# Performance work log

Measured on AMD Instinct MI355X. Metric: run time of the kernel, lower is better.

The kernel has to match this reference:

```python
import jax, jax.numpy as jnp
import numpy as np

N, C, W_DIM, H_DIM = 2, 256, 64, 64
HEADS = 4
DH = C // HEADS  # per-head dim for Q,K,V projections
EPS = 1e-5


def _layernorm(x, w, b):
    mu = jnp.mean(x, axis=-1, keepdims=True)
    var = jnp.var(x, axis=-1, keepdims=True)
    return (x - mu) * jax.lax.rsqrt(var + EPS) * w + b


def setup_inputs() -> dict:
    key = jax.random.key(0)
    ks = jax.random.split(key, 12)
    s = 1.0 / np.sqrt(C)
    return {
        "x": jax.random.normal(ks[0], (N, C, W_DIM, H_DIM), dtype=jnp.float32),
        "ln1_w": jnp.ones((C,), jnp.float32),
        "ln1_b": jnp.zeros((C,), jnp.float32),
        # per-head projection weights, laid out for x @ W: [heads, C, DH]
        "WQ": jax.random.normal(ks[1], (HEADS, C, DH), jnp.float32) * s,
        "WK": jax.random.normal(ks[2], (HEADS, C, DH), jnp.float32) * s,
        "WV": jax.random.normal(ks[3], (HEADS, C, DH), jnp.float32) * s,
        "ln2_w": jnp.ones((C,), jnp.float32),
        "ln2_b": jnp.zeros((C,), jnp.float32),
        "W1": jax.random.normal(ks[4], (C, C), jnp.float32) * s,
        "b1": jnp.zeros((C,), jnp.float32),
        "W2": jax.random.normal(ks[5], (C, C), jnp.float32) * s,
        "b2": jnp.zeros((C,), jnp.float32),
    }


def reference(x, ln1_w, ln1_b, WQ, WK, WV, ln2_w, ln2_b, W1, b1, W2, b2):
    n, c, w, h = x.shape
    s = w * h
    # 'n c w h -> n (w h) c'
    r = x.reshape(n, c, s).transpose(0, 2, 1)          # [n, s, c]
    norm = _layernorm(r, ln1_w, ln1_b)
    # all heads at once (original loops over heads)
    Q = jnp.einsum('nsc,hcd->nhsd', norm, WQ)
    K = jnp.einsum('nsc,hcd->nhsd', norm, WK)
    V = jnp.einsum('nsc,hcd->nhsd', norm, WV)
    # scale is 1/sqrt(seq_len) per original (keys.shape[1])
    y = jnp.einsum('nhqd,nhkd->nhqk', Q, K) / jnp.sqrt(jnp.float32(s))
    # QUIRK: softmax over dim=1 of [n, q, k] => the QUERY axis (axis=2 here)
    z = jax.nn.softmax(y, axis=2)
    attn = jnp.einsum('nhqk,nhkd->nhqd', z, V)         # [n, h, s, dh]
    attn_cat = attn.transpose(0, 2, 1, 3).reshape(n, s, c)
    out = attn_cat + r
    out = _layernorm(out, ln2_w, ln2_b)
    out = jax.nn.gelu(out @ W1 + b1, approximate=False) @ W2 + b2
    out = out + attn_cat
    # 'n (w h) c -> n c w h'
    return out.transpose(0, 2, 1).reshape(n, c, w, h)
```

## Files before the change

kernel.cpp:

```cpp
#include <hip/hip_runtime.h>
#include <math.h>

#define SEQ 4096
#define CH  256
#define NHT 8
#define DHD 64

#define QSCALE 0.0225421092f

using bf16x8 = __attribute__((ext_vector_type(8))) short;
using f32x4  = __attribute__((ext_vector_type(4))) float;
typedef unsigned short u16;
typedef unsigned int   u32;

__device__ __forceinline__ u16 f2bf(float f) {
    u32 u = __float_as_uint(f);
    u = (u + 0x7fffu + ((u >> 16) & 1u)) >> 16;
    return (u16)u;
}
__device__ __forceinline__ float bf2f(u16 h) {
    return __uint_as_float(((u32)h) << 16);
}
__device__ __forceinline__ float fexp2(float x) {
    return __builtin_amdgcn_exp2f(x);
}

__global__ __launch_bounds__(256) void k_prep(const float* __restrict__ x,
                                              const float* __restrict__ ln1w,
                                              const float* __restrict__ ln1b,
                                              const float* __restrict__ WQ,
                                              const float* __restrict__ WK,
                                              const float* __restrict__ WV,
                                              const float* __restrict__ W1,
                                              const float* __restrict__ W2,
                                              u16* __restrict__ norm,
                                              u16* __restrict__ BtQKV,
                                              u16* __restrict__ W1t,
                                              u16* __restrict__ W2t)
{
    __shared__ float tile[32][257];
    __shared__ float mu[32], rs[32];
    int bid = blockIdx.x;
    int t = threadIdx.x;
    if (bid < 1280) {
        int id = bid * 256 + t;
        if (id < 768 * 256) {
            int j = id >> 8, c = id & 255;
            int which = j >> 8, h = (j >> 6) & 3, d = j & 63;
            const float* W = (which == 0) ? WQ : (which == 1) ? WK : WV;
            BtQKV[id] = f2bf(W[(h * 256 + c) * 64 + d]);
        } else if (id < 768 * 256 + 65536) {
            int jj = id - 768 * 256;
            int j = jj >> 8, c = jj & 255;
            W1t[jj] = f2bf(W1[c * 256 + j]);
        } else if (id < 768 * 256 + 2 * 65536) {
            int jj = id - 768 * 256 - 65536;
            int j = jj >> 8, c = jj & 255;
            W2t[jj] = f2bf(W2[c * 256 + j]);
        }
        return;
    }
    int b2i = bid - 1280;
    int n = b2i >> 7, s0 = (b2i & 127) * 32;
    int sl = t & 31, cg = t >> 5;
    for (int cc = 0; cc < 256; cc += 8) {
        int c = cc + cg;
        tile[sl][c] = x[(n * 256 + c) * SEQ + s0 + sl];
    }
    __syncthreads();
    int wv = t >> 6, l = t & 63;
    for (int rr = 0; rr < 8; rr++) {
        int s = wv * 8 + rr;
        float a0 = tile[s][l], a1 = tile[s][l + 64], a2 = tile[s][l + 128], a3 = tile[s][l + 192];
        float sm = a0 + a1 + a2 + a3;
        float sq = a0 * a0 + a1 * a1 + a2 * a2 + a3 * a3;
        for (int off = 32; off; off >>= 1) { sm += __shfl_xor(sm, off); sq += __shfl_xor(sq, off); }
        if (l == 0) {
            float m = sm * (1.f / 256.f);
            mu[s] = m;
            rs[s] = rsqrtf(sq * (1.f / 256.f) - m * m + 1e-5f);
        }
    }
    __syncthreads();
    float ww = ln1w[t], bb = ln1b[t];
    for (int s = 0; s < 32; s++) {
        float v = (tile[s][t] - mu[s]) * rs[s] * ww + bb;
        norm[(n * SEQ + s0 + s) * 256 + t] = f2bf(v);
    }
}

__global__ __launch_bounds__(256) void k_qkv(const u16* __restrict__ norm,
                                             const u16* __restrict__ Bt,
                                             u16* __restrict__ Qo,
                                             u16* __restrict__ Ko,
                                             u16* __restrict__ Vto)
{
    int m0 = blockIdx.x * 64, j0 = blockIdx.y * 128;
    int t = threadIdx.x, w = t >> 6, lane = t & 63, quad = lane >> 4, l16 = lane & 15;
    const u16* Ap = norm + (long)(m0 + w * 16 + l16) * 256;
    const u16* Bp = Bt + (long)j0 * 256;
    f32x4 z = {0.f, 0.f, 0.f, 0.f};
    f32x4 acc[8];
    #pragma unroll
    for (int j = 0; j < 8; j++) acc[j] = z;
    #pragma unroll
    for (int kc = 0; kc < 8; kc++) {
        bf16x8 a = *(const bf16x8*)&Ap[kc * 32 + quad * 8];
        #pragma unroll
        for (int j = 0; j < 8; j++) {
            bf16x8 b = *(const bf16x8*)&Bp[(long)(j * 16 + l16) * 256 + kc * 32 + quad * 8];
            acc[j] = __builtin_amdgcn_mfma_f32_16x16x32_bf16(a, b, acc[j], 0, 0, 0);
        }
    }
    #pragma unroll
    for (int j = 0; j < 8; j++) {
        int col = j0 + j * 16 + l16;
        int which = col >> 8, h = (col >> 6) & 3, d = col & 63;
        int m = m0 + w * 16 + quad * 4;
        int n = m >> 12, s = m & 4095;
        if (which == 2) {
            u16 h0 = f2bf(acc[j][0]), h1 = f2bf(acc[j][1]);
            u16 h2_ = f2bf(acc[j][2]), h3 = f2bf(acc[j][3]);
            uint2 pk;
            pk.x = (u32)h0 | ((u32)h1 << 16);
            pk.y = (u32)h2_ | ((u32)h3 << 16);
            *(uint2*)&Vto[((long)(n * 4 + h) * 64 + d) * SEQ + s] = pk;
        } else {
            u16* dst = (which == 0) ? Qo : Ko;
            float sc = (which == 0) ? QSCALE : 1.0f;
            #pragma unroll
            for (int r = 0; r < 4; r++)
                dst[((n * 4 + h) * SEQ + s + r) * 64 + d] = f2bf(acc[j][r] * sc);
        }
    }
}

__global__ __launch_bounds__(256) void k_pass1(const u16* __restrict__ Q,
                                               const u16* __restrict__ Km,
                                               float* __restrict__ D2)
{
    __shared__ float Dred[128];
    int nh = blockIdx.y, k0 = blockIdx.x * 128, qc = blockIdx.z;
    const u16* Qh = Q + (long)nh * SEQ * 64;
    const u16* Kh = Km + (long)nh * SEQ * 64;
    int t = threadIdx.x, w = t >> 6, lane = t & 63, quad = lane >> 4, l16 = lane & 15;
    bf16x8 Kf[8][2];
    #pragma unroll
    for (int i = 0; i < 8; i++) {
        Kf[i][0] = *(const bf16x8*)&Kh[(k0 + i * 16 + l16) * 64 + quad * 8];
        Kf[i][1] = *(const bf16x8*)&Kh[(k0 + i * 16 + l16) * 64 + 32 + quad * 8];
    }
    if (t < 128) Dred[t] = 0.f;
    f32x4 z = {0.f, 0.f, 0.f, 0.f};
    float Dacc[8][4] = {};
    const int qw0 = qc * 2048 + w * 512;
    bf16x8 b0 = *(const bf16x8*)&Qh[(qw0 + l16) * 64 + quad * 8];
    bf16x8 b1 = *(const bf16x8*)&Qh[(qw0 + l16) * 64 + 32 + quad * 8];
    for (int step = 0; step < 32; step++) {
        int q = qw0 + step * 16;
        bf16x8 n0, n1;
        if (step < 31) {
            n0 = *(const bf16x8*)&Qh[(q + 16 + l16) * 64 + quad * 8];
            n1 = *(const bf16x8*)&Qh[(q + 16 + l16) * 64 + 32 + quad * 8];
        }
        #pragma unroll
        for (int i = 0; i < 8; i++) {
            f32x4 acc = z;
            acc = __builtin_amdgcn_mfma_f32_16x16x32_bf16(Kf[i][0], b0, acc, 0, 0, 0);
            acc = __builtin_amdgcn_mfma_f32_16x16x32_bf16(Kf[i][1], b1, acc, 0, 0, 0);
            #pragma unroll
            for (int r = 0; r < 4; r++) Dacc[i][r] += fexp2(acc[r]);
        }
        b0 = n0; b1 = n1;
    }
    #pragma unroll
    for (int i = 0; i < 8; i++)
        #pragma unroll
        for (int r = 0; r < 4; r++) {
            float v = Dacc[i][r];
            v += __shfl_xor(v, 1); v += __shfl_xor(v, 2);
            v += __shfl_xor(v, 4); v += __shfl_xor(v, 8);
            Dacc[i][r] = v;
        }
    __syncthreads();
    if (l16 == 0) {
        #pragma unroll
        for (int i = 0; i < 8; i++)
            #pragma unroll
            for (int r = 0; r < 4; r++)
                atomicAdd(&Dred[i * 16 + quad * 4 + r], Dacc[i][r]);
    }
    __syncthreads();
    if (t < 128) D2[((long)(qc * NHT + nh)) * SEQ + k0 + t] = Dred[t];
}

__global__ __launch_bounds__(256, 1) void k_pass2(const u16* __restrict__ Q,
                                                  const u16* __restrict__ Km,
                                                  const u16* __restrict__ Vt,
                                                  const float* __restrict__ D2,
                                                  float* __restrict__ acat2)
{
    __shared__ __align__(16) u16 lP[4][128][36];
    __shared__ float Lk[2048];
    float (*red)[68] = (float(*)[68])lP;

    int nh = blockIdx.y, q0 = blockIdx.x * 128, kcid = blockIdx.z;
    int n = nh >> 2, h = nh & 3;
    const u16* Qh = Q + (long)nh * SEQ * 64;
    const u16* Kh = Km + (long)nh * SEQ * 64;
    const u16* Vh = Vt + (long)nh * 64 * SEQ;
    int t = threadIdx.x, w = t >> 6, lane = t & 63, quad = lane >> 4, l16 = lane & 15;
    const int kw0 = kcid * 2048 + w * 512;
    const int klw = w * 512;

    {
        const float* Dp = D2 + (long)nh * SEQ + kcid * 2048;
        const long QS = (long)NHT * SEQ;
        #pragma unroll
        for (int off = 0; off < 8; off++) {
            int kl = off * 256 + t;
            Lk[kl] = __log2f(Dp[kl] + Dp[QS + kl]);
        }
    }
    bf16x8 Qf[8][2];
    #pragma unroll
    for (int jq = 0; jq < 8; jq++)
        #pragma unroll
        for (int ch = 0; ch < 2; ch++)
            Qf[jq][ch] = *(const bf16x8*)&Qh[(q0 + jq * 16 + l16) * 64 + ch * 32 + quad * 8];
    bf16x8 kA[2][2];
    #pragma unroll
    for (int ksub = 0; ksub < 2; ksub++) {
        kA[ksub][0] = *(const bf16x8*)&Kh[(kw0 + ksub * 16 + l16) * 64 + quad * 8];
        kA[ksub][1] = *(const bf16x8*)&Kh[(kw0 + ksub * 16 + l16) * 64 + 32 + quad * 8];
    }
    bf16x8 vb[4];
    #pragma unroll
    for (int jd = 0; jd < 4; jd++)
        vb[jd] = *(const bf16x8*)&Vh[(jd * 16 + l16) * SEQ + kw0 + quad * 8];
    f32x4 z = {0.f, 0.f, 0.f, 0.f};
    f32x4 accO[8][4];
    #pragma unroll
    for (int jq = 0; jq < 8; jq++)
        #pragma unroll
        for (int jd = 0; jd < 4; jd++) accO[jq][jd] = z;
    __syncthreads();

    for (int i = 0; i < 16; i++) {
        int k0 = kw0 + i * 32;
        #pragma unroll
        for (int ksub = 0; ksub < 2; ksub++) {
            f32x4 Lv = *(const f32x4*)&Lk[klw + i * 32 + ksub * 16 + quad * 4];
            #pragma unroll
            for (int jq = 0; jq < 8; jq++) {
                f32x4 acc = z;
                acc = __builtin_amdgcn_mfma_f32_16x16x32_bf16(kA[ksub][0], Qf[jq][0], acc, 0, 0, 0);
                acc = __builtin_amdgcn_mfma_f32_16x16x32_bf16(kA[ksub][1], Qf[jq][1], acc, 0, 0, 0);
                u32 e0 = __float_as_uint(fexp2(acc[0] - Lv[0]));
                u32 e1 = __float_as_uint(fexp2(acc[1] - Lv[1]));
                u32 e2 = __float_as_uint(fexp2(acc[2] - Lv[2]));
                u32 e3 = __float_as_uint(fexp2(acc[3] - Lv[3]));
                uint2 pk;
                pk.x = __builtin_amdgcn_perm(e1, e0, 0x07060302u);
                pk.y = __builtin_amdgcn_perm(e3, e2, 0x07060302u);
                *(uint2*)&lP[w][jq * 16 + l16][ksub * 16 + quad * 4] = pk;
            }
        }
        if (i < 15) {
            #pragma unroll
            for (int ksub = 0; ksub < 2; ksub++) {
                kA[ksub][0] = *(const bf16x8*)&Kh[(k0 + 32 + ksub * 16 + l16) * 64 + quad * 8];
                kA[ksub][1] = *(const bf16x8*)&Kh[(k0 + 32 + ksub * 16 + l16) * 64 + 32 + quad * 8];
            }
        }
        #pragma unroll
        for (int jq = 0; jq < 8; jq++) {
            bf16x8 pa = *(const bf16x8*)&lP[w][jq * 16 + l16][quad * 8];
            #pragma unroll
            for (int jd = 0; jd < 4; jd++)
                accO[jq][jd] = __builtin_amdgcn_mfma_f32_16x16x32_bf16(pa, vb[jd], accO[jq][jd], 0, 0, 0);
        }
        if (i < 15) {
            #pragma unroll
            for (int jd = 0; jd < 4; jd++)
                vb[jd] = *(const bf16x8*)&Vh[(jd * 16 + l16) * SEQ + k0 + 32 + quad * 8];
        }
    }
    __syncthreads();
    for (int src = 0; src < 4; src++) {
        if (w == src) {
            #pragma unroll
            for (int jq = 0; jq < 8; jq++)
                #pragma unroll
                for (int jd = 0; jd < 4; jd++)
                    #pragma unroll
                    for (int r = 0; r < 4; r++) {
                        float* cell = &red[jq * 16 + quad * 4 + r][jd * 16 + l16];
                        if (src == 0) *cell = accO[jq][jd][r];
                        else          *cell += accO[jq][jd][r];
                    }
        }
        __syncthreads();
    }
    float* dst = acat2 + (long)kcid * 8192 * 256;
    #pragma unroll
    for (int p = 0; p < 8; p++) {
        int row = p * 16 + (t >> 4);
        int ch = (t & 15) * 4;
        float4 o = *(float4*)&red[row][ch];
        *(float4*)&dst[((long)n * SEQ + q0 + row) * 256 + h * 64 + ch] = o;
    }
}

__global__ __launch_bounds__(256) void k_tail(const float* __restrict__ x,
                                              const float* __restrict__ acat2,
                                              const float* __restrict__ lnw,
                                              const float* __restrict__ lnb,
                                              const u16* __restrict__ W1t,
                                              const float* __restrict__ b1v,
                                              const u16* __restrict__ W2t,
                                              const float* __restrict__ b2v,
                                              float* __restrict__ out)
{
    __shared__ __align__(16) unsigned char smem[16448];
    float (*tile)[257] = (float(*)[257])smem;
    u16 (*lT)[264] = (u16(*)[264])smem;
    __shared__ float aF[16][257];
    __shared__ float mu[16], rs[16];
    __shared__ __align__(16) u16 lH[16][264];

    const long STRIDE = (long)8192 * 256;
    int m0 = blockIdx.x * 16;
    int n = m0 >> 12, s0 = m0 & 4095;
    int t = threadIdx.x, w = t >> 6, lane = t & 63, quad = lane >> 4, l16 = lane & 15;

    {
        int sl = t & 15, cg = t >> 4;
        for (int cc = 0; cc < 256; cc += 16) {
            int c = cc + cg;
            tile[sl][c] = x[(n * 256 + c) * SEQ + s0 + sl];
        }
    }
    __syncthreads();
    for (int s = 0; s < 16; s++) {
        long idx = (long)(m0 + s) * 256 + t;
        float a = acat2[idx] + acat2[idx + STRIDE];
        aF[s][t] = a;
        tile[s][t] += a;
    }
    __syncthreads();
    {
        int l = t & 63;
        for (int rr = 0; rr < 4; rr++) {
            int s = w * 4 + rr;
            float a0 = tile[s][l], a1 = tile[s][l + 64], a2 = tile[s][l + 128], a3 = tile[s][l + 192];
            float sm = a0 + a1 + a2 + a3;
            float sq = a0 * a0 + a1 * a1 + a2 * a2 + a3 * a3;
            for (int off = 32; off; off >>= 1) { sm += __shfl_xor(sm, off); sq += __shfl_xor(sq, off); }
            if (l == 0) {
                float m = sm * (1.f / 256.f);
                mu[s] = m;
                rs[s] = rsqrtf(sq * (1.f / 256.f) - m * m + 1e-5f);
            }
        }
    }
    __syncthreads();
    {
        float ww = lnw[t], bb = lnb[t];
        for (int s = 0; s < 16; s++)
            lH[s][t] = f2bf((tile[s][t] - mu[s]) * rs[s] * ww + bb);
    }
    __syncthreads();

    f32x4 z = {0.f, 0.f, 0.f, 0.f};
    f32x4 acc1[4];
    #pragma unroll
    for (int js = 0; js < 4; js++) acc1[js] = z;
    #pragma unroll
    for (int kc = 0; kc < 8; kc++) {
        bf16x8 b = *(const bf16x8*)&lH[l16][kc * 32 + quad * 8];
        #pragma unroll
        for (int js = 0; js < 4; js++) {
            bf16x8 a = *(const bf16x8*)&W1t[(long)(w * 64 + js * 16 + l16) * 256 + kc * 32 + quad * 8];
            acc1[js] = __builtin_amdgcn_mfma_f32_16x16x32_bf16(a, b, acc1[js], 0, 0, 0);
        }
    }
    #pragma unroll
    for (int js = 0; js < 4; js++) {
        u32 e[4];
        #pragma unroll
        for (int r = 0; r < 4; r++) {
            int j = w * 64 + js * 16 + quad * 4 + r;
            float v = acc1[js][r] + b1v[j];
            float g = 0.5f * v * (1.f + erff(v * 0.70710678118f));
            u32 u = __float_as_uint(g);
            e[r] = u + 0x7fffu + ((u >> 16) & 1u);
        }
        uint2 pk;
        pk.x = __builtin_amdgcn_perm(e[1], e[0], 0x07060302u);
        pk.y = __builtin_amdgcn_perm(e[3], e[2], 0x07060302u);
        *(uint2*)&lT[l16][w * 64 + js * 16 + quad * 4] = pk;
    }
    __syncthreads();
    f32x4 acc2[4];
    #pragma unroll
    for (int cs = 0; cs < 4; cs++) acc2[cs] = z;
    #pragma unroll
    for (int kc = 0; kc < 8; kc++) {
        bf16x8 pa = *(const bf16x8*)&lT[l16][kc * 32 + quad * 8];
        #pragma unroll
        for (int cs = 0; cs < 4; cs++) {
            bf16x8 wb = *(const bf16x8*)&W2t[(long)(w * 64 + cs * 16 + l16) * 256 + kc * 32 + quad * 8];
            acc2[cs] = __builtin_amdgcn_mfma_f32_16x16x32_bf16(pa, wb, acc2[cs], 0, 0, 0);
        }
    }
    #pragma unroll
    for (int cs = 0; cs < 4; cs++) {
        int c = w * 64 + cs * 16 + l16;
        float bj = b2v[c];
        float vv[4];
        #pragma unroll
        for (int r = 0; r < 4; r++)
            vv[r] = acc2[cs][r] + bj + aF[quad * 4 + r][c];
        float4 o = make_float4(vv[0], vv[1], vv[2], vv[3]);
        *(float4*)&out[((long)n * 256 + c) * SEQ + s0 + quad * 4] = o;
    }
}

extern "C" void kernel_launch(void* const* d_in, const int* in_sizes, int n_in,
                              void* d_out, int out_size, void* d_ws, size_t ws_size,
                              hipStream_t stream) {
    const float* x    = (const float*)d_in[0];
    const float* ln1w = (const float*)d_in[1];
    const float* ln1b = (const float*)d_in[2];
    const float* WQ   = (const float*)d_in[3];
    const float* WK   = (const float*)d_in[4];
    const float* WV   = (const float*)d_in[5];
    const float* ln2w = (const float*)d_in[6];
    const float* ln2b = (const float*)d_in[7];
    const float* W1   = (const float*)d_in[8];
    const float* b1   = (const float*)d_in[9];
    const float* W2   = (const float*)d_in[10];
    const float* b2   = (const float*)d_in[11];
    float* out = (float*)d_out;

    char* p = (char*)d_ws;
    u16* norm   = (u16*)p;   p += (size_t)8192 * 256 * 2;
    u16* BtQKV  = (u16*)p;   p += (size_t)768 * 256 * 2;
    u16* W1t    = (u16*)p;   p += (size_t)256 * 256 * 2;
    u16* W2t    = (u16*)p;   p += (size_t)256 * 256 * 2;
    u16* Qb     = (u16*)p;   p += (size_t)NHT * SEQ * 64 * 2;
    u16* Kb     = (u16*)p;   p += (size_t)NHT * SEQ * 64 * 2;
    u16* VtT    = (u16*)p;   p += (size_t)NHT * SEQ * 64 * 2;
    float* D2   = (float*)p; p += (size_t)2 * NHT * SEQ * 4;
    float* acat2= (float*)p; p += (size_t)2 * 8192 * 256 * 4;

    k_prep<<<1536, 256, 0, stream>>>(x, ln1w, ln1b, WQ, WK, WV, W1, W2,
                                     norm, BtQKV, W1t, W2t);
    k_qkv<<<dim3(128, 6), 256, 0, stream>>>(norm, BtQKV, Qb, Kb, VtT);
    k_pass1<<<dim3(32, 8, 2), 256, 0, stream>>>(Qb, Kb, D2);
    k_pass2<<<dim3(32, 8, 2), 256, 0, stream>>>(Qb, Kb, VtT, D2, acat2);
    k_tail<<<512, 256, 0, stream>>>(x, acat2, ln2w, ln2b, W1t, b1, W2t, b2, out);
}
```

Measured before the change: 232.1 us.

## Double-buffer P tile and software-pipeline QK/exp with PV MFMAs in pass2

Splits the per-wave P staging buffer in LDS into two buffers. The loop is restructured so the QK MFMA plus exp phase for step i+1 is issued before the PV MFMA phase for step i. This aims to overlap the exp2/pack VALU work and the LDS writes with independent matrix-core work, rather than serialising them within each step. The cost is doubled LDS use for P and a longer, fully unrolled code body.

```diff
diff --git a/kernel.cpp b/kernel.cpp
--- a/kernel.cpp
+++ b/kernel.cpp
@@ -200,9 +200,10 @@
                                                   const float* __restrict__ D2,
                                                   float* __restrict__ acat2)
 {
-    __shared__ __align__(16) u16 lP[4][128][36];
+    __shared__ __align__(16) u16 lPA[4][128][36];
+    __shared__ __align__(16) u16 lPB[4][128][36];
     __shared__ float Lk[2048];
-    float (*red)[68] = (float(*)[68])lP;
+    float (*red)[68] = (float(*)[68])lPA;
 
     int nh = blockIdx.y, q0 = blockIdx.x * 128, kcid = blockIdx.z;
     int n = nh >> 2, h = nh & 3;
@@ -246,46 +247,70 @@
         for (int jd = 0; jd < 4; jd++) accO[jq][jd] = z;
     __syncthreads();
 
-    for (int i = 0; i < 16; i++) {
-        int k0 = kw0 + i * 32;
-        #pragma unroll
-        for (int ksub = 0; ksub < 2; ksub++) {
-            f32x4 Lv = *(const f32x4*)&Lk[klw + i * 32 + ksub * 16 + quad * 4];
-            #pragma unroll
-            for (int jq = 0; jq < 8; jq++) {
-                f32x4 acc = z;
-                acc = __builtin_amdgcn_mfma_f32_16x16x32_bf16(kA[ksub][0], Qf[jq][0], acc, 0, 0, 0);
-                acc = __builtin_amdgcn_mfma_f32_16x16x32_bf16(kA[ksub][1], Qf[jq][1], acc, 0, 0, 0);
-                u32 e0 = __float_as_uint(fexp2(acc[0] - Lv[0]));
-                u32 e1 = __float_as_uint(fexp2(acc[1] - Lv[1]));
-                u32 e2 = __float_as_uint(fexp2(acc[2] - Lv[2]));
-                u32 e3 = __float_as_uint(fexp2(acc[3] - Lv[3]));
-                uint2 pk;
-                pk.x = __builtin_amdgcn_perm(e1, e0, 0x07060302u);
-                pk.y = __builtin_amdgcn_perm(e3, e2, 0x07060302u);
-                *(uint2*)&lP[w][jq * 16 + l16][ksub * 16 + quad * 4] = pk;
-            }
-        }
-        if (i < 15) {
-            #pragma unroll
-            for (int ksub = 0; ksub < 2; ksub++) {
-                kA[ksub][0] = *(const bf16x8*)&Kh[(k0 + 32 + ksub * 16 + l16) * 64 + quad * 8];
-                kA[ksub][1] = *(const bf16x8*)&Kh[(k0 + 32 + ksub * 16 + l16) * 64 + 32 + quad * 8];
-            }
-        }
-        #pragma unroll
-        for (int jq = 0; jq < 8; jq++) {
-            bf16x8 pa = *(const bf16x8*)&lP[w][jq * 16 + l16][quad * 8];
-            #pragma unroll
-            for (int jd = 0; jd < 4; jd++)
-                accO[jq][jd] = __builtin_amdgcn_mfma_f32_16x16x32_bf16(pa, vb[jd], accO[jq][jd], 0, 0, 0);
-        }
-        if (i < 15) {
-            #pragma unroll
-            for (int jd = 0; jd < 4; jd++)
-                vb[jd] = *(const bf16x8*)&Vh[(jd * 16 + l16) * SEQ + k0 + 32 + quad * 8];
-        }
-    }
+#define QK_PHASE(I, LPD)                                                      \
+    {                                                                         \
+        const int _i = (I);                                                   \
+        _Pragma("unroll")                                                     \
+        for (int ksub = 0; ksub < 2; ksub++) {                                \
+            f32x4 Lv = *(const f32x4*)&Lk[klw + _i * 32 + ksub * 16 + quad * 4]; \
+            _Pragma("unroll")                                                 \
+            for (int jq = 0; jq < 8; jq++) {                                  \
+                f32x4 acc = z;                                                \
+                acc = __builtin_amdgcn_mfma_f32_16x16x32_bf16(kA[ksub][0], Qf[jq][0], acc, 0, 0, 0); \
+                acc = __builtin_amdgcn_mfma_f32_16x16x32_bf16(kA[ksub][1], Qf[jq][1], acc, 0, 0, 0); \
+                u32 e0 = __float_as_uint(fexp2(acc[0] - Lv[0]));              \
+                u32 e1 = __float_as_uint(fexp2(acc[1] - Lv[1]));              \
+                u32 e2 = __float_as_uint(fexp2(acc[2] - Lv[2]));              \
+                u32 e3 = __float_as_uint(fexp2(acc[3] - Lv[3]));              \
+                uint2 pk;                                                     \
+                pk.x = __builtin_amdgcn_perm(e1, e0, 0x07060302u);            \
+                pk.y = __builtin_amdgcn_perm(e3, e2, 0x07060302u);            \
+                *(uint2*)&LPD[w][jq * 16 + l16][ksub * 16 + quad * 4] = pk;   \
+            }                                                                 \
+        }                                                                     \
+        if (_i < 15) {                                                        \
+            int kn = kw0 + _i * 32 + 32;                                      \
+            _Pragma("unroll")                                                 \
+            for (int ksub = 0; ksub < 2; ksub++) {                            \
+                kA[ksub][0] = *(const bf16x8*)&Kh[(kn + ksub * 16 + l16) * 64 + quad * 8]; \
+                kA[ksub][1] = *(const bf16x8*)&Kh[(kn + ksub * 16 + l16) * 64 + 32 + quad * 8]; \
+            }                                                                 \
+        }                                                                     \
+    }
+
+#define PV_PHASE(I, LPS)                                                      \
+    {                                                                         \
+        const int _i = (I);                                                   \
+        _Pragma("unroll")                                                     \
+        for (int jq = 0; jq < 8; jq++) {                                      \
+            bf16x8 pa = *(const bf16x8*)&LPS[w][jq * 16 + l16][quad * 8];     \
+            _Pragma("unroll")                                                 \
+            for (int jd = 0; jd < 4; jd++)                                    \
+                accO[jq][jd] = __builtin_amdgcn_mfma_f32_16x16x32_bf16(pa, vb[jd], accO[jq][jd], 0, 0, 0); \
+        }                                                                     \
+        if (_i < 15) {                                                        \
+            int kn = kw0 + _i * 32 + 32;                                      \
+            _Pragma("unroll")                                                 \
+            for (int jd = 0; jd < 4; jd++)                                    \
+                vb[jd] = *(const bf16x8*)&Vh[(jd * 16 + l16) * SEQ + kn + quad * 8]; \
+        }                                                                     \
+    }
+
+    QK_PHASE(0, lPA)
+    for (int tt = 0; tt < 7; tt++) {
+        int i = tt * 2;
+        QK_PHASE(i + 1, lPB)
+        PV_PHASE(i,     lPA)
+        QK_PHASE(i + 2, lPA)
+        PV_PHASE(i + 1, lPB)
+    }
+    QK_PHASE(15, lPB)
+    PV_PHASE(14, lPA)
+    PV_PHASE(15, lPB)
+
+#undef QK_PHASE
+#undef PV_PHASE
+
     __syncthreads();
     for (int src = 0; src < 4; src++) {
         if (w == src) {
```

Result: slower. 237.1 us (+2.2%).
